# Performance work log

Measured on AMD Instinct MI355X. Metric: run time of the kernel, lower is better.

Reference implementation:

```python
import jax, jax.numpy as jnp
import numpy as np

N_NODES = 50000
N_SCHEMES = 5
K = 16
HIDDEN = 128
N_CLASSES = 8


def setup_inputs() -> dict:
    key = jax.random.key(0)
    ks = jax.random.split(key, 8)
    sc_nei = jax.random.randint(ks[0], (N_SCHEMES, N_NODES, K), 0, N_NODES)
    feats = jax.random.normal(ks[1], (N_NODES, HIDDEN), dtype=jnp.float32)
    W1 = jax.random.normal(ks[2], (HIDDEN, HIDDEN), dtype=jnp.float32) * (1.0 / np.sqrt(HIDDEN))
    b1 = jnp.zeros((HIDDEN,), dtype=jnp.float32)
    W2 = jax.random.normal(ks[3], (HIDDEN, N_CLASSES), dtype=jnp.float32) * (1.0 / np.sqrt(HIDDEN))
    b2 = jnp.zeros((N_CLASSES,), dtype=jnp.float32)
    alpha = jax.random.normal(ks[4], (N_NODES, 1), dtype=jnp.float32)
    attention = jax.random.normal(ks[5], (N_NODES, N_SCHEMES, 1), dtype=jnp.float32)
    return {"sc_nei": sc_nei, "feats": feats, "W1": W1, "b1": b1,
            "W2": W2, "b2": b2, "alpha": alpha, "attention": attention}


def _mlp(x, W1, b1, W2, b2):
    # MLP2 with num_layers=2, dropout in eval mode (identity)
    h = jax.nn.relu(x @ W1 + b1)
    return h @ W2 + b2


def reference(sc_nei, feats, W1, b1, W2, b2, alpha, attention):
    # Per-scheme: gather -> MLP -> exp(log_softmax)=softmax -> mean over neighbors
    emb = feats[sc_nei]                      # [5, N, K, H]
    probs = jax.nn.softmax(_mlp(emb, W1, b1, W2, b2), axis=-1)  # [5, N, K, C]
    sc_cls = probs.mean(axis=2)              # [5, N, C]
    x = jnp.moveaxis(sc_cls, 0, -1)          # [N, C, 5]
    att = jax.nn.softmax(attention, axis=1)  # [N, 5, 1]
    scheme_pred = jnp.squeeze(x @ att, -1)   # [N, C]
    self_pred = jax.nn.softmax(_mlp(feats[:N_NODES], W1, b1, W2, b2), axis=-1)  # [N, C]
    gate = jax.nn.sigmoid(alpha)             # sigmoid(-a) = 1 - sigmoid(a)
    return gate * self_pred + (1.0 - gate) * scheme_pred
```

## Files before the change

### kernel.cpp

```cpp
#include <hip/hip_runtime.h>
#include <hip/hip_bf16.h>
#include <math.h>

#define HIDDEN   128
#define NCLS     8
#define NSCHEMES 5
#define KNEI     16

typedef __attribute__((ext_vector_type(8))) short short8;
typedef __attribute__((ext_vector_type(4))) float floatx4;

static __device__ inline unsigned pk2(float x, float y) {
    __hip_bfloat162 v = __float22bfloat162_rn(float2{x, y});
    union { __hip_bfloat162 b; unsigned u; } cv; cv.b = v;
    return cv.u;
}

__global__ __launch_bounds__(256) void convert_w1(
    const float* __restrict__ W1, unsigned short* __restrict__ W1T)
{
    int idx = blockIdx.x * 256 + threadIdx.x;
    int j = idx & 127, k = idx >> 7;
    unsigned u = __float_as_uint(W1[k * HIDDEN + j]);
    u = (u + 0x7fffu + ((u >> 16) & 1u)) >> 16;
    W1T[j * HIDDEN + k] = (unsigned short)u;
}

__global__ __launch_bounds__(256) void mlp_mfma(
    const float* __restrict__ feats, const unsigned short* __restrict__ W1T,
    const float* __restrict__ b1, const float* __restrict__ W2,
    const float* __restrict__ b2, float* __restrict__ probs, int N)
{
    const int lane = threadIdx.x & 63;
    const int wv   = threadIdx.x >> 6;
    const int quad = lane >> 4;
    const int l16  = lane & 15;
    const int nodeBase = blockIdx.x * 64 + wv * 16;

    int myNode = nodeBase + l16;
    if (myNode >= N) myNode = N - 1;

    floatx4 acc[8];
    #pragma unroll
    for (int t = 0; t < 8; ++t) acc[t] = (floatx4){0.f, 0.f, 0.f, 0.f};

    const float* arow = feats + (size_t)myNode * HIDDEN + quad * 8;
    #pragma unroll
    for (int c = 0; c < 4; ++c) {
        float4 a0 = *(const float4*)(arow + c * 32);
        float4 a1 = *(const float4*)(arow + c * 32 + 4);
        union { short8 s; unsigned u[4]; } af;
        af.u[0] = pk2(a0.x, a0.y);
        af.u[1] = pk2(a0.z, a0.w);
        af.u[2] = pk2(a1.x, a1.y);
        af.u[3] = pk2(a1.z, a1.w);
        #pragma unroll
        for (int t = 0; t < 8; ++t) {
            short8 bf = *(const short8*)(W1T + (size_t)(t * 16 + l16) * HIDDEN
                                               + c * 32 + quad * 8);
            acc[t] = __builtin_amdgcn_mfma_f32_16x16x32_bf16(af.s, bf, acc[t], 0, 0, 0);
        }
    }

    float opart[4][NCLS];
    #pragma unroll
    for (int r = 0; r < 4; ++r)
        #pragma unroll
        for (int c = 0; c < NCLS; ++c) opart[r][c] = 0.f;

    #pragma unroll
    for (int t = 0; t < 8; ++t) {
        int j = t * 16 + l16;
        float bj = b1[j];
        float4 w0 = *(const float4*)(W2 + j * NCLS);
        float4 w1 = *(const float4*)(W2 + j * NCLS + 4);
        #pragma unroll
        for (int r = 0; r < 4; ++r) {
            float h = fmaxf(acc[t][r] + bj, 0.f);
            opart[r][0] = fmaf(h, w0.x, opart[r][0]);
            opart[r][1] = fmaf(h, w0.y, opart[r][1]);
            opart[r][2] = fmaf(h, w0.z, opart[r][2]);
            opart[r][3] = fmaf(h, w0.w, opart[r][3]);
            opart[r][4] = fmaf(h, w1.x, opart[r][4]);
            opart[r][5] = fmaf(h, w1.y, opart[r][5]);
            opart[r][6] = fmaf(h, w1.z, opart[r][6]);
            opart[r][7] = fmaf(h, w1.w, opart[r][7]);
        }
    }

    #pragma unroll
    for (int r = 0; r < 4; ++r)
        #pragma unroll
        for (int c = 0; c < NCLS; ++c) {
            float v = opart[r][c];
            v += __shfl_xor(v, 1, 64);
            v += __shfl_xor(v, 2, 64);
            v += __shfl_xor(v, 4, 64);
            v += __shfl_xor(v, 8, 64);
            opart[r][c] = v;
        }

    if (l16 == 0) {
        float4 b2lo = *(const float4*)b2;
        float4 b2hi = *(const float4*)(b2 + 4);
        float bb[NCLS] = {b2lo.x, b2lo.y, b2lo.z, b2lo.w, b2hi.x, b2hi.y, b2hi.z, b2hi.w};
        #pragma unroll
        for (int r = 0; r < 4; ++r) {
            int n = nodeBase + quad * 4 + r;
            if (n < N) {
                float o[NCLS];
                #pragma unroll
                for (int c = 0; c < NCLS; ++c) o[c] = opart[r][c] + bb[c];
                float m = o[0];
                #pragma unroll
                for (int c = 1; c < NCLS; ++c) m = fmaxf(m, o[c]);
                float s = 0.f;
                #pragma unroll
                for (int c = 0; c < NCLS; ++c) { o[c] = __expf(o[c] - m); s += o[c]; }
                float inv = 1.f / s;
                float4* op = (float4*)(probs + (size_t)n * NCLS);
                op[0] = make_float4(o[0] * inv, o[1] * inv, o[2] * inv, o[3] * inv);
                op[1] = make_float4(o[4] * inv, o[5] * inv, o[6] * inv, o[7] * inv);
            }
        }
    }
}

__global__ __launch_bounds__(256) void combine(
    const int* __restrict__ nei, const float* __restrict__ probs,
    const float* __restrict__ attention, const float* __restrict__ alpha,
    float* __restrict__ out, int N)
{
    int t = blockIdx.x * 256 + threadIdx.x;
    int n = t >> 3;
    int L = t & 7;
    if (n >= N) return;

    float aw[NSCHEMES];
    float m = -1e30f;
    #pragma unroll
    for (int s = 0; s < NSCHEMES; ++s) {
        aw[s] = attention[(size_t)n * NSCHEMES + s];
        m = fmaxf(m, aw[s]);
    }
    float ssum = 0.f;
    #pragma unroll
    for (int s = 0; s < NSCHEMES; ++s) { aw[s] = __expf(aw[s] - m); ssum += aw[s]; }

    float g = 1.f / (1.f + __expf(-alpha[n]));
    float scale = (1.f - g) / (ssum * (float)KNEI);
    float wn[NSCHEMES];
    #pragma unroll
    for (int s = 0; s < NSCHEMES; ++s) wn[s] = aw[s] * scale;

    float acc[NCLS];
    #pragma unroll
    for (int c = 0; c < NCLS; ++c) acc[c] = 0.f;

    #pragma unroll
    for (int mm = 0; mm < 10; ++mm) {
        int s = mm >> 1;
        int k = ((mm & 1) << 3) + L;
        int id = nei[((size_t)s * N + n) * KNEI + k];
        const float4* pp = (const float4*)(probs + (size_t)id * NCLS);
        float4 p0 = pp[0], p1 = pp[1];
        float w = wn[s];
        acc[0] = fmaf(w, p0.x, acc[0]);
        acc[1] = fmaf(w, p0.y, acc[1]);
        acc[2] = fmaf(w, p0.z, acc[2]);
        acc[3] = fmaf(w, p0.w, acc[3]);
        acc[4] = fmaf(w, p1.x, acc[4]);
        acc[5] = fmaf(w, p1.y, acc[5]);
        acc[6] = fmaf(w, p1.z, acc[6]);
        acc[7] = fmaf(w, p1.w, acc[7]);
    }

    #pragma unroll
    for (int c = 0; c < NCLS; ++c) {
        float v = acc[c];
        v += __shfl_xor(v, 1, 64);
        v += __shfl_xor(v, 2, 64);
        v += __shfl_xor(v, 4, 64);
        acc[c] = v;
    }

    float self = probs[(size_t)n * NCLS + L];
    float res = acc[0];
    #pragma unroll
    for (int c = 1; c < NCLS; ++c) res = (L == c) ? acc[c] : res;
    out[t] = fmaf(g, self, res);
}

extern "C" void kernel_launch(void* const* d_in, const int* in_sizes, int n_in,
                              void* d_out, int out_size, void* d_ws, size_t ws_size,
                              hipStream_t stream) {
    const int*   sc_nei    = (const int*)d_in[0];
    const float* feats     = (const float*)d_in[1];
    const float* W1        = (const float*)d_in[2];
    const float* b1        = (const float*)d_in[3];
    const float* W2        = (const float*)d_in[4];
    const float* b2        = (const float*)d_in[5];
    const float* alpha     = (const float*)d_in[6];
    const float* attention = (const float*)d_in[7];
    float* out = (float*)d_out;

    int N = in_sizes[1] / HIDDEN;

    float* probs = (float*)d_ws;
    unsigned short* W1T = (unsigned short*)((float*)d_ws + (size_t)N * NCLS);

    convert_w1<<<(HIDDEN * HIDDEN) / 256, 256, 0, stream>>>(W1, W1T);
    mlp_mfma<<<(N + 63) / 64, 256, 0, stream>>>(feats, W1T, b1, W2, b2, probs, N);
    combine<<<((N * NCLS) + 255) / 256, 256, 0, stream>>>(sc_nei, probs, attention, alpha, out, N);
}
```

Baseline: 132.6 us.

## Store probs as bf16, prelayout W1 into MFMA fragments staged in LDS

W1 is converted once into an MFMA-fragment-ordered bf16 layout, and each MLP block copies it into shared memory together with W2 and b1, replacing per-wave global loads of weights. The intermediate per-node probability table is written and gathered as bf16 (16 bytes per node instead of 32), halving the random-gather traffic in the combine kernel. This costs 32KB+ of LDS per block, which may limit occupancy, plus a block-wide sync. It also lowers the precision of the stored probabilities.

```diff
diff --git a/kernel.cpp b/kernel.cpp
--- a/kernel.cpp
+++ b/kernel.cpp
@@ -6,6 +6,7 @@
 #define NCLS     8
 #define NSCHEMES 5
 #define KNEI     16
+#define NFRAG    2048
 
 typedef __attribute__((ext_vector_type(8))) short short8;
 typedef __attribute__((ext_vector_type(4))) float floatx4;
@@ -15,27 +16,55 @@
     union { __hip_bfloat162 b; unsigned u; } cv; cv.b = v;
     return cv.u;
 }
+static __device__ inline float bf2f(unsigned short u) {
+    return __uint_as_float(((unsigned)u) << 16);
+}
 
 __global__ __launch_bounds__(256) void convert_w1(
-    const float* __restrict__ W1, unsigned short* __restrict__ W1T)
+    const float* __restrict__ W1, unsigned short* __restrict__ W1frag)
 {
-    int idx = blockIdx.x * 256 + threadIdx.x;
-    int j = idx & 127, k = idx >> 7;
-    unsigned u = __float_as_uint(W1[k * HIDDEN + j]);
-    u = (u + 0x7fffu + ((u >> 16) & 1u)) >> 16;
-    W1T[j * HIDDEN + k] = (unsigned short)u;
-}
-
-__global__ __launch_bounds__(256) void mlp_mfma(
-    const float* __restrict__ feats, const unsigned short* __restrict__ W1T,
+    int f = blockIdx.x * 256 + threadIdx.x;
+    int lane = f & 63, c = (f >> 6) & 3, t = f >> 8;
+    int q = lane >> 4, l16 = lane & 15;
+    int j  = t * 16 + l16;
+    int k0 = c * 32 + q * 8;
+    union { short8 s; unsigned u[4]; } r;
+    #pragma unroll
+    for (int p = 0; p < 4; ++p) {
+        float a = W1[(size_t)(k0 + 2 * p)     * HIDDEN + j];
+        float b = W1[(size_t)(k0 + 2 * p + 1) * HIDDEN + j];
+        r.u[p] = pk2(a, b);
+    }
+    *(short8*)(W1frag + (size_t)f * 8) = r.s;
+}
+
+__global__ __launch_bounds__(256, 4) void mlp_mfma(
+    const float* __restrict__ feats, const unsigned short* __restrict__ W1frag,
     const float* __restrict__ b1, const float* __restrict__ W2,
-    const float* __restrict__ b2, float* __restrict__ probs, int N)
+    const float* __restrict__ b2, unsigned short* __restrict__ probsb, int N)
 {
-    const int lane = threadIdx.x & 63;
-    const int wv   = threadIdx.x >> 6;
+    __shared__ unsigned short fragLds[NFRAG * 8];
+    __shared__ float W2l[HIDDEN * NCLS];
+    __shared__ float b1l[HIDDEN];
+
+    const int tid  = threadIdx.x;
+    const int lane = tid & 63;
+    const int wv   = tid >> 6;
     const int quad = lane >> 4;
     const int l16  = lane & 15;
     const int nodeBase = blockIdx.x * 64 + wv * 16;
+
+    #pragma unroll
+    for (int it = 0; it < 8; ++it) {
+        short8 v = *(const short8*)(W1frag + (size_t)(it * 256 + tid) * 8);
+        *(short8*)&fragLds[(it * 256 + tid) * 8] = v;
+    }
+    {
+        float4 v = ((const float4*)W2)[tid];
+        *(float4*)&W2l[4 * tid] = v;
+    }
+    if (tid < HIDDEN) b1l[tid] = b1[tid];
+    __syncthreads();
 
     int myNode = nodeBase + l16;
     if (myNode >= N) myNode = N - 1;
@@ -56,8 +85,7 @@
         af.u[3] = pk2(a1.z, a1.w);
         #pragma unroll
         for (int t = 0; t < 8; ++t) {
-            short8 bf = *(const short8*)(W1T + (size_t)(t * 16 + l16) * HIDDEN
-                                               + c * 32 + quad * 8);
+            short8 bf = *(const short8*)&fragLds[((t * 4 + c) * 64 + lane) * 8];
             acc[t] = __builtin_amdgcn_mfma_f32_16x16x32_bf16(af.s, bf, acc[t], 0, 0, 0);
         }
     }
@@ -71,9 +99,9 @@
     #pragma unroll
     for (int t = 0; t < 8; ++t) {
         int j = t * 16 + l16;
-        float bj = b1[j];
-        float4 w0 = *(const float4*)(W2 + j * NCLS);
-        float4 w1 = *(const float4*)(W2 + j * NCLS + 4);
+        float bj = b1l[j];
+        float4 w0 = *(const float4*)&W2l[j * NCLS];
+        float4 w1 = *(const float4*)&W2l[j * NCLS + 4];
         #pragma unroll
         for (int r = 0; r < 4; ++r) {
             float h = fmaxf(acc[t][r] + bj, 0.f);
@@ -118,16 +146,19 @@
                 #pragma unroll
                 for (int c = 0; c < NCLS; ++c) { o[c] = __expf(o[c] - m); s += o[c]; }
                 float inv = 1.f / s;
-                float4* op = (float4*)(probs + (size_t)n * NCLS);
-                op[0] = make_float4(o[0] * inv, o[1] * inv, o[2] * inv, o[3] * inv);
-                op[1] = make_float4(o[4] * inv, o[5] * inv, o[6] * inv, o[7] * inv);
+                union { short8 s8; unsigned u[4]; } pr;
+                pr.u[0] = pk2(o[0] * inv, o[1] * inv);
+                pr.u[1] = pk2(o[2] * inv, o[3] * inv);
+                pr.u[2] = pk2(o[4] * inv, o[5] * inv);
+                pr.u[3] = pk2(o[6] * inv, o[7] * inv);
+                *(short8*)(probsb + (size_t)n * NCLS) = pr.s8;
             }
         }
     }
 }
 
 __global__ __launch_bounds__(256) void combine(
-    const int* __restrict__ nei, const float* __restrict__ probs,
+    const int* __restrict__ nei, const unsigned short* __restrict__ probsb,
     const float* __restrict__ attention, const float* __restrict__ alpha,
     float* __restrict__ out, int N)
 {
@@ -162,17 +193,11 @@
         int s = mm >> 1;
         int k = ((mm & 1) << 3) + L;
         int id = nei[((size_t)s * N + n) * KNEI + k];
-        const float4* pp = (const float4*)(probs + (size_t)id * NCLS);
-        float4 p0 = pp[0], p1 = pp[1];
+        short8 pr = *(const short8*)(probsb + (size_t)id * NCLS);
         float w = wn[s];
-        acc[0] = fmaf(w, p0.x, acc[0]);
-        acc[1] = fmaf(w, p0.y, acc[1]);
-        acc[2] = fmaf(w, p0.z, acc[2]);
-        acc[3] = fmaf(w, p0.w, acc[3]);
-        acc[4] = fmaf(w, p1.x, acc[4]);
-        acc[5] = fmaf(w, p1.y, acc[5]);
-        acc[6] = fmaf(w, p1.z, acc[6]);
-        acc[7] = fmaf(w, p1.w, acc[7]);
+        #pragma unroll
+        for (int c = 0; c < NCLS; ++c)
+            acc[c] = fmaf(w, bf2f((unsigned short)pr[c]), acc[c]);
     }
 
     #pragma unroll
@@ -184,7 +209,7 @@
         acc[c] = v;
     }
 
-    float self = probs[(size_t)n * NCLS + L];
+    float self = bf2f(probsb[(size_t)n * NCLS + L]);
     float res = acc[0];
     #pragma unroll
     for (int c = 1; c < NCLS; ++c) res = (L == c) ? acc[c] : res;
@@ -206,10 +231,10 @@
 
     int N = in_sizes[1] / HIDDEN;
 
-    float* probs = (float*)d_ws;
-    unsigned short* W1T = (unsigned short*)((float*)d_ws + (size_t)N * NCLS);
-
-    convert_w1<<<(HIDDEN * HIDDEN) / 256, 256, 0, stream>>>(W1, W1T);
-    mlp_mfma<<<(N + 63) / 64, 256, 0, stream>>>(feats, W1T, b1, W2, b2, probs, N);
-    combine<<<((N * NCLS) + 255) / 256, 256, 0, stream>>>(sc_nei, probs, attention, alpha, out, N);
-}
+    unsigned short* probsb = (unsigned short*)d_ws;
+    unsigned short* W1frag = (unsigned short*)d_ws + (size_t)N * NCLS;
+
+    convert_w1<<<NFRAG / 256, 256, 0, stream>>>(W1, W1frag);
+    mlp_mfma<<<(N + 63) / 64, 256, 0, stream>>>(feats, W1frag, b1, W2, b2, probsb, N);
+    combine<<<((N * NCLS) + 255) / 256, 256, 0, stream>>>(sc_nei, probsb, attention, alpha, out, N);
+}
```

Result: faster. 121.8 us (-8.1%).
